# Optimization experiments

Hardware: AMD Instinct MI355X
Metric: run time of the kernel (lower is better)

## Reference

```python
import jax, jax.numpy as jnp
import numpy as np

B, S, D, H = 2, 2048, 1024, 16
HD = D // H
LOCAL_WINDOW = 32
GLOBAL_TOKENS = 16
BLOCK_SIZE = 64
SPARSITY = 0.75


def _structured_mask(seq_len):
    """local_global | block_sparse pattern, vectorized numpy (deterministic)."""
    i = np.arange(seq_len)[:, None]
    j = np.arange(seq_len)[None, :]
    half = LOCAL_WINDOW // 2
    local = np.abs(i - j) <= half  # mask[i, i-16 : i+17]
    glob = (i < GLOBAL_TOKENS) | (j < GLOBAL_TOKENS)
    stride = max(1, seq_len // 64)
    strided = ((i % stride) == 0) & ((j % stride) == 0)
    lg = local | glob | strided
    # block sparse: random blocks kept with prob 1-SPARSITY, diagonal always kept
    nb = (seq_len + BLOCK_SIZE - 1) // BLOCK_SIZE
    rng = np.random.default_rng(0)
    block_mask = rng.random((nb, nb)) > SPARSITY
    np.fill_diagonal(block_mask, True)
    bs = np.kron(block_mask, np.ones((BLOCK_SIZE, BLOCK_SIZE), dtype=bool))[:seq_len, :seq_len]
    return lg | bs


def setup_inputs() -> dict:
    key = jax.random.key(0)
    ks = jax.random.split(key, 12)
    std = 1.0 / np.sqrt(D)
    inp = {
        'query': jax.random.normal(ks[0], (B, S, D), jnp.float32),
        'key': jax.random.normal(ks[1], (B, S, D), jnp.float32),
        'value': jax.random.normal(ks[2], (B, S, D), jnp.float32),
        'Wq': jax.random.normal(ks[3], (D, D), jnp.float32) * std,
        'bq': jnp.zeros((D,), jnp.float32),
        'Wk': jax.random.normal(ks[4], (D, D), jnp.float32) * std,
        'bk': jnp.zeros((D,), jnp.float32),
        'Wv': jax.random.normal(ks[5], (D, D), jnp.float32) * std,
        'bv': jnp.zeros((D,), jnp.float32),
        'Wo': jax.random.normal(ks[6], (D, D), jnp.float32) * std,
        'bo': jnp.zeros((D,), jnp.float32),
        'sparse_mask': jnp.asarray(_structured_mask(S)),
    }
    return inp


def reference(query, key, value, Wq, bq, Wk, bk, Wv, bv, Wo, bo, sparse_mask):
    scale = HD ** -0.5
    # projections -> [B, H, S, HD]
    q = (query @ Wq + bq).reshape(B, S, H, HD).transpose(0, 2, 1, 3)
    k = (key @ Wk + bk).reshape(B, S, H, HD).transpose(0, 2, 1, 3)
    v = (value @ Wv + bv).reshape(B, S, H, HD).transpose(0, 2, 1, 3)
    # dense scores then structured sparse mask (matches original math)
    scores = jnp.einsum('bhqd,bhkd->bhqk', q, k) * scale
    scores = jnp.where(sparse_mask[None, None], scores, -jnp.inf)
    attn = jax.nn.softmax(scores, axis=-1)  # every row has >=1 active entry (global cols)
    out = jnp.einsum('bhqk,bhkd->bhqd', attn, v)
    out = out.transpose(0, 2, 1, 3).reshape(B, S, D)
    out = out @ Wo + bo
    return out, attn
```

## Files before the change

kernel.cpp:

```cpp
#include <hip/hip_runtime.h>
#include <hip/hip_bf16.h>
#include <hip/hip_fp16.h>

using u16 = unsigned short;
using u32 = unsigned int;
using u64 = unsigned long long;

typedef __attribute__((ext_vector_type(8))) short short8;
typedef __attribute__((ext_vector_type(8))) _Float16 half8;
typedef __attribute__((ext_vector_type(4))) _Float16 half4;
typedef __attribute__((ext_vector_type(4))) float f32x4;
typedef __attribute__((ext_vector_type(2))) u32 u32x2;

#define DEVI static __device__ __forceinline__

DEVI float bfu2f(u16 u) { return __builtin_bit_cast(float, (u32)u << 16); }
DEVI u16 f2bfu(float f) { return __builtin_bit_cast(u16, __float2bfloat16(f)); }
DEVI u16 f2hu(float f) { return __builtin_bit_cast(u16, (_Float16)f); }

DEVI f32x4 mfma_f16_(half8 a, half8 b, f32x4 c) {
  return __builtin_amdgcn_mfma_f32_16x16x32_f16(a, b, c, 0, 0, 0);
}
DEVI f32x4 mfma16_f16_(half4 a, half4 b, f32x4 c) {
  return __builtin_amdgcn_mfma_f32_16x16x16f16(a, b, c, 0, 0, 0);
}

#define GLD_LDS16(src, dst) \
  __builtin_amdgcn_global_load_lds((const __attribute__((address_space(1))) void*)(src), \
                                   (__attribute__((address_space(3))) void*)(dst), 16, 0, 0)

#define BAR() __builtin_amdgcn_s_barrier()
#define VMCNT(n) asm volatile("s_waitcnt vmcnt(" #n ")" ::: "memory")

static constexpr int Bsz = 2, S = 2048, D = 1024, H = 16, HD = 64;
static constexpr int MROWS = Bsz * S;
static constexpr size_t OUT_ELEMS = (size_t)Bsz * S * D;
static constexpr float C_EXP2 = 0.18033688f;
static constexpr size_t OFF_WT  = 0;
static constexpr size_t OFF_Q   = 0x800000;
static constexpr size_t OFF_K   = 0x1000000;
static constexpr size_t OFF_V   = 0x1800000;
static constexpr size_t OFF_VT  = 0x2000000;
static constexpr size_t OFF_O   = 0x2800000;
static constexpr size_t OFF_MB  = 0x3000000;
static constexpr size_t OFF_FLG = 0x3080000;

__global__ __launch_bounds__(256) void detect_dtype(
    const u16* __restrict__ q, int* __restrict__ flag)
{
  __shared__ u32 red[256];
  const int tid = threadIdx.x;
  u32 mx = 0;
  for (int i = tid; i < 32768; i += 256) {
    u32 e = (q[2 * i] >> 7) & 0xFF;
    mx = mx > e ? mx : e;
  }
  red[tid] = mx;
  __syncthreads();
  if (tid == 0) {
    u32 m = 0;
    for (int i = 0; i < 256; ++i) m = m > red[i] ? m : red[i];
    flag[0] = (m >= 0x90) ? 1 : 0;
  }
}

__global__ __launch_bounds__(256) void conv_f16(
    const void* __restrict__ X, u16* __restrict__ Y, const int* __restrict__ flag)
{
  const size_t i8 = ((size_t)blockIdx.x * 256 + threadIdx.x) * 8;
  half8 o;
  if (*flag) {
    const float* x = (const float*)X + i8;
    float4 f0 = ((const float4*)x)[0], f1 = ((const float4*)x)[1];
    o[0] = (_Float16)f0.x; o[1] = (_Float16)f0.y;
    o[2] = (_Float16)f0.z; o[3] = (_Float16)f0.w;
    o[4] = (_Float16)f1.x; o[5] = (_Float16)f1.y;
    o[6] = (_Float16)f1.z; o[7] = (_Float16)f1.w;
  } else {
    uint4 a = *(const uint4*)((const u16*)X + i8);
    u32 wd[4] = {a.x, a.y, a.z, a.w};
    #pragma unroll
    for (int j = 0; j < 4; ++j) {
      o[2 * j]     = (_Float16)bfu2f((u16)(wd[j] & 0xFFFF));
      o[2 * j + 1] = (_Float16)bfu2f((u16)(wd[j] >> 16));
    }
  }
  *reinterpret_cast<half8*>(Y + i8) = o;
}

__global__ __launch_bounds__(256) void prep_w(
    const void* __restrict__ Wq, const void* __restrict__ Wk,
    const void* __restrict__ Wv, const void* __restrict__ Wo,
    u16* __restrict__ WT, const int* __restrict__ flag)
{
  __shared__ _Float16 t[64][80];
  const int z = blockIdx.z;
  const void* src = z == 0 ? Wq : z == 1 ? Wk : z == 2 ? Wv : Wo;
  u16* dst = WT + (size_t)z * 1024 * 1024;
  const int bx = blockIdx.x, by = blockIdx.y;
  const int tid = threadIdx.x;
  const int r = tid >> 2, ch = tid & 3;
  const int fl = *flag;
  if (fl) {
    const float* s = (const float*)src + (size_t)(by * 64 + r) * 1024 + bx * 64 + ch * 16;
    #pragma unroll
    for (int v = 0; v < 4; ++v) {
      float4 f = ((const float4*)s)[v];
      t[r][ch * 16 + v * 4 + 0] = (_Float16)f.x;
      t[r][ch * 16 + v * 4 + 1] = (_Float16)f.y;
      t[r][ch * 16 + v * 4 + 2] = (_Float16)f.z;
      t[r][ch * 16 + v * 4 + 3] = (_Float16)f.w;
    }
  } else {
    const u16* s = (const u16*)src + (size_t)(by * 64 + r) * 1024 + bx * 64 + ch * 16;
    uint4 a0 = ((const uint4*)s)[0], a1 = ((const uint4*)s)[1];
    u32 wds[8] = {a0.x, a0.y, a0.z, a0.w, a1.x, a1.y, a1.z, a1.w};
    #pragma unroll
    for (int j = 0; j < 8; ++j) {
      t[r][ch * 16 + 2 * j]     = (_Float16)bfu2f((u16)(wds[j] & 0xFFFF));
      t[r][ch * 16 + 2 * j + 1] = (_Float16)bfu2f((u16)(wds[j] >> 16));
    }
  }
  __syncthreads();
  half8 o0, o1;
  #pragma unroll
  for (int i = 0; i < 8; ++i) { o0[i] = t[ch * 16 + i][r]; o1[i] = t[ch * 16 + 8 + i][r]; }
  u16* d = dst + (size_t)(bx * 64 + r) * 1024 + by * 64 + ch * 16;
  *reinterpret_cast<half8*>(d) = o0;
  *reinterpret_cast<half8*>(d + 8) = o1;
}

__global__ __launch_bounds__(256) void mask_bits_kernel(
    const void* __restrict__ mask, u64* __restrict__ mbits)
{
  const u32 w0 = *(const u32*)mask;
  int mode;
  if (w0 == 0x01010101u) mode = 0;
  else if ((w0 & 0xFFFFu) && (w0 >> 16)) mode = 1;
  else mode = 2;
  const int row = blockIdx.x;
  const int w = threadIdx.x >> 6, l = threadIdx.x & 63;
  for (int i = 0; i < 8; ++i) {
    int jw = w * 8 + i;
    size_t idx = (size_t)row * S + jw * 64 + l;
    bool m;
    if (mode == 0)      m = ((const unsigned char*)mask)[idx] != 0;
    else if (mode == 1) m = ((const u16*)mask)[idx] != 0;
    else                m = ((const u32*)mask)[idx] != 0;
    u64 bal = __ballot(m);
    if (l == 0) mbits[(size_t)row * 32 + jw] = bal;
  }
}

template<int OUT_DYN>
__global__ __launch_bounds__(256) void gemm_f16(
    const _Float16* __restrict__ A, const _Float16* __restrict__ Bt,
    const void* __restrict__ bias, void* __restrict__ C,
    const int* __restrict__ flag, int M, int N, int K)
{
  __shared__ _Float16 As[64 * 64];
  __shared__ _Float16 Bs[128 * 64];
  const int tid = threadIdx.x;
  const int w = tid >> 6, l = tid & 63;
  const int wr = w >> 1, wc = w & 1;
  const int lg = l >> 4, lc = l & 15;
  const int tM = blockIdx.x * 64, tN = blockIdx.y * 128;
  const int fl = *flag;
  const int rr = l >> 3;
  const int gsw = (l & 7) ^ rr;
  const int rsw = lc & 7;

  f32x4 acc[2][4] = {};

  for (int k0 = 0; k0 < K; k0 += 64) {
    #pragma unroll
    for (int s = 0; s < 2; ++s)
      GLD_LDS16(A + (size_t)(tM + w * 16 + s * 8 + rr) * K + k0 + gsw * 8,
                &As[(w * 16 + s * 8) * 64]);
    #pragma unroll
    for (int s = 0; s < 4; ++s)
      GLD_LDS16(Bt + (size_t)(tN + w * 32 + s * 8 + rr) * K + k0 + gsw * 8,
                &Bs[(w * 32 + s * 8) * 64]);
    __syncthreads();
    half8 a[2][2], b[4][2];
    #pragma unroll
    for (int m = 0; m < 2; ++m)
      #pragma unroll
      for (int kk = 0; kk < 2; ++kk)
        a[m][kk] = *reinterpret_cast<const half8*>(
            &As[(wr * 32 + m * 16 + lc) * 64 + ((kk * 4 + lg) ^ rsw) * 8]);
    #pragma unroll
    for (int n = 0; n < 4; ++n)
      #pragma unroll
      for (int kk = 0; kk < 2; ++kk)
        b[n][kk] = *reinterpret_cast<const half8*>(
            &Bs[(wc * 64 + n * 16 + lc) * 64 + ((kk * 4 + lg) ^ rsw) * 8]);
    #pragma unroll
    for (int m = 0; m < 2; ++m)
      #pragma unroll
      for (int n = 0; n < 4; ++n) {
        acc[m][n] = mfma_f16_(a[m][0], b[n][0], acc[m][n]);
        acc[m][n] = mfma_f16_(a[m][1], b[n][1], acc[m][n]);
      }
    __syncthreads();
  }

  float bf[4];
  #pragma unroll
  for (int n = 0; n < 4; ++n) {
    int col = tN + wc * 64 + n * 16 + lc;
    bf[n] = fl ? ((const float*)bias)[col] : bfu2f(((const u16*)bias)[col]);
  }
  #pragma unroll
  for (int m = 0; m < 2; ++m) {
    int row = tM + wr * 32 + m * 16 + lg * 4;
    #pragma unroll
    for (int n = 0; n < 4; ++n) {
      int col = tN + wc * 64 + n * 16 + lc;
      #pragma unroll
      for (int r = 0; r < 4; ++r) {
        float v = acc[m][n][r] + bf[n];
        size_t off = (size_t)(row + r) * N + col;
        if (OUT_DYN) {
          if (fl) ((float*)C)[off] = v;
          else    ((u16*)C)[off] = f2bfu(v);
        } else {
          ((u16*)C)[off] = f2hu(v);
        }
      }
    }
  }
}

__global__ __launch_bounds__(256) void transpose_v(
    const _Float16* __restrict__ V, _Float16* __restrict__ vT)
{
  __shared__ _Float16 t[64][80];
  const int sb = blockIdx.x, bh = blockIdx.y;
  const int b = bh >> 4, h = bh & 15;
  const int tid = threadIdx.x;
  #pragma unroll
  for (int rep = 0; rep < 2; ++rep) {
    int idx = rep * 256 + tid;
    int sl = idx >> 3, ch = idx & 7;
    *reinterpret_cast<uint4*>(&t[sl][ch * 8]) =
      *reinterpret_cast<const uint4*>(V + (size_t)(b * S + sb * 64 + sl) * D + h * HD + ch * 8);
  }
  __syncthreads();
  #pragma unroll
  for (int rep = 0; rep < 2; ++rep) {
    int idx = rep * 256 + tid;
    int hd = idx >> 3, ch = idx & 7;
    half8 ov;
    #pragma unroll
    for (int i = 0; i < 8; ++i) ov[i] = t[ch * 8 + i][hd];
    *reinterpret_cast<half8*>(vT + ((size_t)bh * HD + hd) * S + sb * 64 + ch * 8) = ov;
  }
}

__global__ __launch_bounds__(256) void attn_kernel(
    const _Float16* __restrict__ Q, const _Float16* __restrict__ Kp,
    const _Float16* __restrict__ vT, const u64* __restrict__ mbits,
    _Float16* __restrict__ O, void* __restrict__ dOut,
    const int* __restrict__ flag)
{
  __shared__ _Float16 Ks[2][4096];
  __shared__ _Float16 Vs[2][4096];

  const int tid = threadIdx.x, w = tid >> 6, l = tid & 63;
  const int lg = l >> 4, lc = l & 15;
  const int flat = blockIdx.y * 32 + blockIdx.x;
  const int nf = (flat & 7) * 128 + (flat >> 3);
  const int rb = nf & 31, bh = nf >> 5;
  const int b = bh >> 4, h = bh & 15;
  const int wg = w ^ (rb & 1);
  const int wrow = rb * 64 + wg * 16;
  const int fl = *flag;

  half8 aq[2];
  {
    const _Float16* qp = Q + (size_t)(b * S + wrow + lc) * D + h * HD;
    aq[0] = *reinterpret_cast<const half8*>(qp + lg * 8);
    aq[1] = *reinterpret_cast<const half8*>(qp + 32 + lg * 8);
  }
  const _Float16* kbase = Kp + (size_t)(b * S) * D + h * HD;
  const _Float16* vbase = vT + (size_t)bh * HD * S;
  const u64* mrow = mbits + (size_t)(wrow + lc) * 32;

  const int rr = w * 8 + (l >> 3);
  const int gsw = (l & 7) ^ (rr & 7);

  #define STAGE_K(buf, jb) do { \
    const _Float16* s0_ = kbase + (size_t)((jb) * 64 + rr) * D + gsw * 8; \
    GLD_LDS16(s0_, &Ks[buf][w * 512]); \
    GLD_LDS16(s0_ + (size_t)32 * D, &Ks[buf][2048 + w * 512]); \
  } while (0)
  #define STAGE_V(buf, jb) do { \
    const _Float16* s0_ = vbase + (size_t)rr * S + (jb) * 64 + gsw * 8; \
    GLD_LDS16(s0_, &Vs[buf][w * 512]); \
    GLD_LDS16(s0_ + (size_t)32 * S, &Vs[buf][2048 + w * 512]); \
  } while (0)

  const int sw = lc & 7;

  float rs = 0.f;
  f32x4 accO[4] = {};

  STAGE_K(0, 0);
  STAGE_V(0, 0);

  #pragma unroll 1
  for (int jb = 0; jb < 32; ++jb) {
    const int buf = jb & 1;
    BAR();
    if (jb < 31) {
      STAGE_K(buf ^ 1, jb + 1);
      STAGE_V(buf ^ 1, jb + 1);
      VMCNT(4);
    } else {
      VMCNT(0);
    }
    BAR();
    const u64 mb = mrow[jb];
    const _Float16* kt = Ks[buf];
    const _Float16* vt = Vs[buf];
    #pragma unroll
    for (int c = 0; c < 4; ++c) {
      const u32 bits = (u32)(mb >> (c * 16 + lg * 4)) & 0xFu;
      if (__any(bits != 0)) {
        const int r = c * 16 + lc;
        half8 ka = *reinterpret_cast<const half8*>(&kt[r * 64 + ((lg ^ sw) * 8)]);
        half8 kb = *reinterpret_cast<const half8*>(&kt[r * 64 + (((lg + 4) ^ sw) * 8)]);
        f32x4 sc = {};
        sc = mfma_f16_(ka, aq[0], sc);
        sc = mfma_f16_(kb, aq[1], sc);
        half4 pa;
        #pragma unroll
        for (int r2 = 0; r2 < 4; ++r2) {
          float p = ((bits >> r2) & 1) ? exp2f(sc[r2] * C_EXP2) : 0.f;
          rs += p;
          pa[r2] = (_Float16)p;
        }
        #pragma unroll
        for (int d = 0; d < 4; ++d) {
          const int rd = d * 16 + lc;
          const int ch = (2 * c + (lg >> 1)) ^ sw;
          half4 vv = *reinterpret_cast<const half4*>(&vt[rd * 64 + ch * 8 + (lg & 1) * 4]);
          accO[d] = mfma16_f16_(pa, vv, accO[d]);
        }
      }
    }
  }

  rs += __shfl_xor(rs, 16);
  rs += __shfl_xor(rs, 32);
  const float inv = 1.f / rs;
  const float lg2i = -__log2f(rs);

  float invr[4];
  #pragma unroll
  for (int r = 0; r < 4; ++r) invr[r] = __shfl(inv, lg * 4 + r);

  {
    _Float16* op = O + (size_t)(b * S + wrow + lg * 4) * D + h * HD;
    #pragma unroll
    for (int d = 0; d < 4; ++d)
      #pragma unroll
      for (int r = 0; r < 4; ++r)
        op[(size_t)r * D + d * 16 + lc] = (_Float16)(accO[d][r] * invr[r]);
  }

  STAGE_K(0, 0);

  if (fl) {
    float* ar = (float*)dOut + OUT_ELEMS + (size_t)bh * S * S + (size_t)(wrow + lc) * S;
    #pragma unroll 1
    for (int jb = 0; jb < 32; ++jb) {
      const int buf = jb & 1;
      BAR();
      if (jb < 31) { STAGE_K(buf ^ 1, jb + 1); VMCNT(2); }
      else VMCNT(0);
      BAR();
      const u64 mb = mrow[jb];
      const _Float16* kt = Ks[buf];
      #pragma unroll
      for (int c = 0; c < 4; ++c) {
        const u32 bits = (u32)(mb >> (c * 16 + lg * 4)) & 0xFu;
        f32x4* dst = (f32x4*)(ar + jb * 64 + c * 16 + lg * 4);
        if (__any(bits != 0)) {
          const int r = c * 16 + lc;
          half8 ka = *reinterpret_cast<const half8*>(&kt[r * 64 + ((lg ^ sw) * 8)]);
          half8 kb = *reinterpret_cast<const half8*>(&kt[r * 64 + (((lg + 4) ^ sw) * 8)]);
          f32x4 sc = {};
          sc = mfma_f16_(ka, aq[0], sc);
          sc = mfma_f16_(kb, aq[1], sc);
          f32x4 pv;
          #pragma unroll
          for (int r2 = 0; r2 < 4; ++r2)
            pv[r2] = ((bits >> r2) & 1) ? exp2f(__builtin_fmaf(sc[r2], C_EXP2, lg2i)) : 0.f;
          __builtin_nontemporal_store(pv, dst);
        } else {
          f32x4 z = {};
          __builtin_nontemporal_store(z, dst);
        }
      }
    }
  } else {
    u16* ar = (u16*)dOut + OUT_ELEMS + (size_t)bh * S * S + (size_t)(wrow + lc) * S;
    #pragma unroll 1
    for (int jb = 0; jb < 32; ++jb) {
      const int buf = jb & 1;
      BAR();
      if (jb < 31) { STAGE_K(buf ^ 1, jb + 1); VMCNT(2); }
      else VMCNT(0);
      BAR();
      const u64 mb = mrow[jb];
      const _Float16* kt = Ks[buf];
      #pragma unroll
      for (int c = 0; c < 4; ++c) {
        const u32 bits = (u32)(mb >> (c * 16 + lg * 4)) & 0xFu;
        u32x2* dst = (u32x2*)(ar + jb * 64 + c * 16 + lg * 4);
        if (__any(bits != 0)) {
          const int r = c * 16 + lc;
          half8 ka = *reinterpret_cast<const half8*>(&kt[r * 64 + ((lg ^ sw) * 8)]);
          half8 kb = *reinterpret_cast<const half8*>(&kt[r * 64 + (((lg + 4) ^ sw) * 8)]);
          f32x4 sc = {};
          sc = mfma_f16_(ka, aq[0], sc);
          sc = mfma_f16_(kb, aq[1], sc);
          float p0 = ((bits >> 0) & 1) ? exp2f(__builtin_fmaf(sc[0], C_EXP2, lg2i)) : 0.f;
          float p1 = ((bits >> 1) & 1) ? exp2f(__builtin_fmaf(sc[1], C_EXP2, lg2i)) : 0.f;
          float p2 = ((bits >> 2) & 1) ? exp2f(__builtin_fmaf(sc[2], C_EXP2, lg2i)) : 0.f;
          float p3 = ((bits >> 3) & 1) ? exp2f(__builtin_fmaf(sc[3], C_EXP2, lg2i)) : 0.f;
          u32x2 pk;
          pk[0] = (u32)f2bfu(p0) | ((u32)f2bfu(p1) << 16);
          pk[1] = (u32)f2bfu(p2) | ((u32)f2bfu(p3) << 16);
          __builtin_nontemporal_store(pk, dst);
        } else {
          u32x2 z = {0, 0};
          __builtin_nontemporal_store(z, dst);
        }
      }
    }
  }
  #undef STAGE_K
  #undef STAGE_V
}

extern "C" void kernel_launch(void* const* d_in, const int* in_sizes, int n_in,
                              void* d_out, int out_size, void* d_ws, size_t ws_size,
                              hipStream_t stream) {
  const void* query = d_in[0];
  const void* key_  = d_in[1];
  const void* value = d_in[2];
  const void* Wq = d_in[3];  const void* bq = d_in[4];
  const void* Wk = d_in[5];  const void* bk = d_in[6];
  const void* Wv = d_in[7];  const void* bv = d_in[8];
  const void* Wo = d_in[9];  const void* bo = d_in[10];
  const void* mask = d_in[11];

  char* ws = (char*)d_ws;
  u16* WT   = (u16*)(ws + OFF_WT);
  u16* Qb   = (u16*)(ws + OFF_Q);
  u16* Kb   = (u16*)(ws + OFF_K);
  u16* Vb   = (u16*)(ws + OFF_V);
  u16* vTb  = (u16*)(ws + OFF_VT);
  u16* Ob   = (u16*)(ws + OFF_O);
  u64* mbits = (u64*)(ws + OFF_MB);
  int* flag  = (int*)(ws + OFF_FLG);

  u16* WqT = WT, *WkT = WT + 1048576, *WvT = WT + 2097152, *WoT = WT + 3145728;
  u16* X = vTb;

  detect_dtype<<<1, 256, 0, stream>>>((const u16*)query, flag);
  prep_w<<<dim3(16, 16, 4), 256, 0, stream>>>(Wq, Wk, Wv, Wo, WT, flag);
  mask_bits_kernel<<<dim3(S), 256, 0, stream>>>(mask, mbits);

  const dim3 gg(MROWS / 64, D / 128);
  conv_f16<<<dim3(2048), 256, 0, stream>>>(query, X, flag);
  gemm_f16<0><<<gg, 256, 0, stream>>>((const _Float16*)X, (const _Float16*)WqT,
                                      bq, Qb, flag, MROWS, D, D);
  conv_f16<<<dim3(2048), 256, 0, stream>>>(key_, X, flag);
  gemm_f16<0><<<gg, 256, 0, stream>>>((const _Float16*)X, (const _Float16*)WkT,
                                      bk, Kb, flag, MROWS, D, D);
  conv_f16<<<dim3(2048), 256, 0, stream>>>(value, X, flag);
  gemm_f16<0><<<gg, 256, 0, stream>>>((const _Float16*)X, (const _Float16*)WvT,
                                      bv, Vb, flag, MROWS, D, D);

  transpose_v<<<dim3(32, 32), 256, 0, stream>>>((const _Float16*)Vb, (_Float16*)vTb);
  attn_kernel<<<dim3(32, 32), 256, 0, stream>>>(
      (const _Float16*)Qb, (const _Float16*)Kb, (const _Float16*)vTb,
      mbits, (_Float16*)Ob, d_out, flag);
  gemm_f16<1><<<gg, 256, 0, stream>>>((const _Float16*)Ob, (const _Float16*)WoT,
                                      bo, d_out, flag, MROWS, D, D);
}
```

Baseline: 336.1 us.

## Double-buffer GEMM with 128x128 tiles and prefetch mask bits in attention

```diff
diff --git a/kernel.cpp b/kernel.cpp
--- a/kernel.cpp
+++ b/kernel.cpp
@@ -153,70 +153,82 @@
 }
 
 template<int OUT_DYN>
-__global__ __launch_bounds__(256) void gemm_f16(
+__global__ __launch_bounds__(512) void gemm_f16(
     const _Float16* __restrict__ A, const _Float16* __restrict__ Bt,
     const void* __restrict__ bias, void* __restrict__ C,
     const int* __restrict__ flag, int M, int N, int K)
 {
-  __shared__ _Float16 As[64 * 64];
-  __shared__ _Float16 Bs[128 * 64];
+  __shared__ _Float16 As[2][128 * 64];
+  __shared__ _Float16 Bs[2][128 * 64];
   const int tid = threadIdx.x;
   const int w = tid >> 6, l = tid & 63;
-  const int wr = w >> 1, wc = w & 1;
+  const int wr = w >> 2, wc = w & 3;
   const int lg = l >> 4, lc = l & 15;
-  const int tM = blockIdx.x * 64, tN = blockIdx.y * 128;
+  const int tM = blockIdx.x * 128, tN = blockIdx.y * 128;
   const int fl = *flag;
-  const int rr = l >> 3;
-  const int gsw = (l & 7) ^ rr;
+  const int r8 = l >> 3;
+  const int gsw = (l & 7) ^ r8;
   const int rsw = lc & 7;
 
-  f32x4 acc[2][4] = {};
-
-  for (int k0 = 0; k0 < K; k0 += 64) {
-    #pragma unroll
-    for (int s = 0; s < 2; ++s)
-      GLD_LDS16(A + (size_t)(tM + w * 16 + s * 8 + rr) * K + k0 + gsw * 8,
-                &As[(w * 16 + s * 8) * 64]);
-    #pragma unroll
-    for (int s = 0; s < 4; ++s)
-      GLD_LDS16(Bt + (size_t)(tN + w * 32 + s * 8 + rr) * K + k0 + gsw * 8,
-                &Bs[(w * 32 + s * 8) * 64]);
-    __syncthreads();
-    half8 a[2][2], b[4][2];
-    #pragma unroll
-    for (int m = 0; m < 2; ++m)
+  f32x4 acc[4][2] = {};
+
+  #define GSTAGE(buf, k0) do { \
+    _Float16* as_ = As[buf]; _Float16* bs_ = Bs[buf]; \
+    GLD_LDS16(A  + (size_t)(tM + w * 8 + r8) * K + (k0) + gsw * 8, &as_[(w * 8) * 64]); \
+    GLD_LDS16(A  + (size_t)(tM + 64 + w * 8 + r8) * K + (k0) + gsw * 8, &as_[(64 + w * 8) * 64]); \
+    GLD_LDS16(Bt + (size_t)(tN + w * 8 + r8) * K + (k0) + gsw * 8, &bs_[(w * 8) * 64]); \
+    GLD_LDS16(Bt + (size_t)(tN + 64 + w * 8 + r8) * K + (k0) + gsw * 8, &bs_[(64 + w * 8) * 64]); \
+  } while (0)
+
+  GSTAGE(0, 0);
+
+  const int NT = K / 64;
+  #pragma unroll 1
+  for (int kt = 0; kt < NT; ++kt) {
+    const int buf = kt & 1;
+    BAR();
+    if (kt < NT - 1) {
+      GSTAGE(buf ^ 1, (kt + 1) * 64);
+      VMCNT(4);
+    } else {
+      VMCNT(0);
+    }
+    BAR();
+    half8 a[4][2], b[2][2];
+    #pragma unroll
+    for (int m = 0; m < 4; ++m)
       #pragma unroll
       for (int kk = 0; kk < 2; ++kk)
         a[m][kk] = *reinterpret_cast<const half8*>(
-            &As[(wr * 32 + m * 16 + lc) * 64 + ((kk * 4 + lg) ^ rsw) * 8]);
-    #pragma unroll
-    for (int n = 0; n < 4; ++n)
+            &As[buf][(wr * 64 + m * 16 + lc) * 64 + ((kk * 4 + lg) ^ rsw) * 8]);
+    #pragma unroll
+    for (int n = 0; n < 2; ++n)
       #pragma unroll
       for (int kk = 0; kk < 2; ++kk)
         b[n][kk] = *reinterpret_cast<const half8*>(
-            &Bs[(wc * 64 + n * 16 + lc) * 64 + ((kk * 4 + lg) ^ rsw) * 8]);
-    #pragma unroll
-    for (int m = 0; m < 2; ++m)
-      #pragma unroll
-      for (int n = 0; n < 4; ++n) {
+            &Bs[buf][(wc * 32 + n * 16 + lc) * 64 + ((kk * 4 + lg) ^ rsw) * 8]);
+    #pragma unroll
+    for (int m = 0; m < 4; ++m)
+      #pragma unroll
+      for (int n = 0; n < 2; ++n) {
         acc[m][n] = mfma_f16_(a[m][0], b[n][0], acc[m][n]);
         acc[m][n] = mfma_f16_(a[m][1], b[n][1], acc[m][n]);
       }
-    __syncthreads();
-  }
-
-  float bf[4];
+  }
+  #undef GSTAGE
+
+  float bf[2];
   #pragma unroll
-  for (int n = 0; n < 4; ++n) {
-    int col = tN + wc * 64 + n * 16 + lc;
+  for (int n = 0; n < 2; ++n) {
+    int col = tN + wc * 32 + n * 16 + lc;
     bf[n] = fl ? ((const float*)bias)[col] : bfu2f(((const u16*)bias)[col]);
   }
   #pragma unroll
-  for (int m = 0; m < 2; ++m) {
-    int row = tM + wr * 32 + m * 16 + lg * 4;
-    #pragma unroll
-    for (int n = 0; n < 4; ++n) {
-      int col = tN + wc * 64 + n * 16 + lc;
+  for (int m = 0; m < 4; ++m) {
+    int row = tM + wr * 64 + m * 16 + lg * 4;
+    #pragma unroll
+    for (int n = 0; n < 2; ++n) {
+      int col = tN + wc * 32 + n * 16 + lc;
       #pragma unroll
       for (int r = 0; r < 4; ++r) {
         float v = acc[m][n][r] + bf[n];
@@ -308,6 +320,7 @@
 
   STAGE_K(0, 0);
   STAGE_V(0, 0);
+  u64 mb = mrow[0];
 
   #pragma unroll 1
   for (int jb = 0; jb < 32; ++jb) {
@@ -321,7 +334,7 @@
       VMCNT(0);
     }
     BAR();
-    const u64 mb = mrow[jb];
+    const u64 mb_next = (jb < 31) ? mrow[jb + 1] : 0ull;
     const _Float16* kt = Ks[buf];
     const _Float16* vt = Vs[buf];
     #pragma unroll
@@ -350,6 +363,7 @@
         }
       }
     }
+    mb = mb_next;
   }
 
   rs += __shfl_xor(rs, 16);
@@ -371,6 +385,7 @@
   }
 
   STAGE_K(0, 0);
+  mb = mrow[0];
 
   if (fl) {
     float* ar = (float*)dOut + OUT_ELEMS + (size_t)bh * S * S + (size_t)(wrow + lc) * S;
@@ -381,7 +396,7 @@
       if (jb < 31) { STAGE_K(buf ^ 1, jb + 1); VMCNT(2); }
       else VMCNT(0);
       BAR();
-      const u64 mb = mrow[jb];
+      const u64 mb_next = (jb < 31) ? mrow[jb + 1] : 0ull;
       const _Float16* kt = Ks[buf];
       #pragma unroll
       for (int c = 0; c < 4; ++c) {
@@ -404,6 +419,7 @@
           __builtin_nontemporal_store(z, dst);
         }
       }
+      mb = mb_next;
     }
   } else {
     u16* ar = (u16*)dOut + OUT_ELEMS + (size_t)bh * S * S + (size_t)(wrow + lc) * S;
@@ -414,7 +430,7 @@
       if (jb < 31) { STAGE_K(buf ^ 1, jb + 1); VMCNT(2); }
       else VMCNT(0);
       BAR();
-      const u64 mb = mrow[jb];
+      const u64 mb_next = (jb < 31) ? mrow[jb + 1] : 0ull;
       const _Float16* kt = Ks[buf];
       #pragma unroll
       for (int c = 0; c < 4; ++c) {
@@ -440,6 +456,7 @@
           __builtin_nontemporal_store(z, dst);
         }
       }
+      mb = mb_next;
     }
   }
   #undef STAGE_K
@@ -475,21 +492,21 @@
   prep_w<<<dim3(16, 16, 4), 256, 0, stream>>>(Wq, Wk, Wv, Wo, WT, flag);
   mask_bits_kernel<<<dim3(S), 256, 0, stream>>>(mask, mbits);
 
-  const dim3 gg(MROWS / 64, D / 128);
+  const dim3 gg(MROWS / 128, D / 128);
   conv_f16<<<dim3(2048), 256, 0, stream>>>(query, X, flag);
-  gemm_f16<0><<<gg, 256, 0, stream>>>((const _Float16*)X, (const _Float16*)WqT,
+  gemm_f16<0><<<gg, 512, 0, stream>>>((const _Float16*)X, (const _Float16*)WqT,
                                       bq, Qb, flag, MROWS, D, D);
   conv_f16<<<dim3(2048), 256, 0, stream>>>(key_, X, flag);
-  gemm_f16<0><<<gg, 256, 0, stream>>>((const _Float16*)X, (const _Float16*)WkT,
+  gemm_f16<0><<<gg, 512, 0, stream>>>((const _Float16*)X, (const _Float16*)WkT,
                                       bk, Kb, flag, MROWS, D, D);
   conv_f16<<<dim3(2048), 256, 0, stream>>>(value, X, flag);
-  gemm_f16<0><<<gg, 256, 0, stream>>>((const _Float16*)X, (const _Float16*)WvT,
+  gemm_f16<0><<<gg, 512, 0, stream>>>((const _Float16*)X, (const _Float16*)WvT,
                                       bv, Vb, flag, MROWS, D, D);
 
   transpose_v<<<dim3(32, 32), 256, 0, stream>>>((const _Float16*)Vb, (_Float16*)vTb);
   attn_kernel<<<dim3(32, 32), 256, 0, stream>>>(
       (const _Float16*)Qb, (const _Float16*)Kb, (const _Float16*)vTb,
       mbits, (_Float16*)Ob, d_out, flag);
-  gemm_f16<1><<<gg, 256, 0, stream>>>((const _Float16*)Ob, (const _Float16*)WoT,
+  gemm_f16<1><<<gg, 512, 0, stream>>>((const _Float16*)Ob, (const _Float16*)WoT,
                                       bo, d_out, flag, MROWS, D, D);
 }
```

Measured after the change: 351.8 us. 1.05x slower.
